# Kernel tuning notes

Measured on AMD Instinct MI355X. Metric: run time of the kernel, lower is better.

Reference implementation:

```python
import jax, jax.numpy as jnp
import numpy as np

B = 4096
D = 256
TEMP = 0.5


def setup_inputs() -> dict:
    key = jax.random.key(0)
    k1, k2 = jax.random.split(key)
    x_i = jax.random.normal(k1, (B, D), dtype=jnp.float32)
    x_j = jax.random.normal(k2, (B, D), dtype=jnp.float32)
    return {"x_i": x_i, "x_j": x_j}


def reference(x_i, x_j):
    b = x_i.shape[0]
    # L2-normalize rows (F.normalize with default eps=1e-12)
    def l2norm(x):
        n = jnp.linalg.norm(x, axis=1, keepdims=True)
        return x / jnp.maximum(n, 1e-12)

    z = jnp.concatenate([l2norm(x_i), l2norm(x_j)], axis=0)  # [2B, D]
    # rows of z are unit-norm, so cosine similarity == dot product
    sim = z @ z.T  # [2B, 2B]

    # positives: diagonals at offsets +B and -B
    idx = jnp.arange(b)
    sim_ij = sim[idx, idx + b]
    sim_ji = sim[idx + b, idx]
    pos = jnp.concatenate([sim_ij, sim_ji], axis=0)  # [2B]

    nom = jnp.exp(pos / TEMP)
    neg_mask = 1.0 - jnp.eye(2 * b, dtype=sim.dtype)
    denom = jnp.sum(neg_mask * jnp.exp(sim / TEMP), axis=1)  # [2B]
    loss = jnp.sum(-jnp.log(nom / denom)) / (2 * b)
    return loss
```

## Files before the change

kernel.cpp:

```cpp
#include <hip/hip_runtime.h>

#define NB   4096
#define ND   256
#define N2B  8192
#define INV_T 2.0f

typedef __attribute__((ext_vector_type(8))) short bf16x8;
typedef __attribute__((ext_vector_type(16))) float f32x16;

__device__ __forceinline__ void gload_lds16(const void* g, void* l) {
  __builtin_amdgcn_global_load_lds(
      (const __attribute__((address_space(1))) void*)g,
      (__attribute__((address_space(3))) void*)l, 16, 0, 0);
}

__device__ __forceinline__ unsigned short f2b(float f) {
  unsigned int u = __float_as_uint(f);
  u = (u + 0x7fffu + ((u >> 16) & 1u)) >> 16;
  return (unsigned short)u;
}
__device__ __forceinline__ float b2f(unsigned short h) {
  return __uint_as_float(((unsigned int)h) << 16);
}

__global__ __launch_bounds__(256) void k_normalize(
    const float* __restrict__ xi, const float* __restrict__ xj,
    unsigned short* __restrict__ Z, float* __restrict__ diagE,
    float* __restrict__ pos, float* __restrict__ lossAcc,
    unsigned int* __restrict__ ticket) {
  __shared__ float sh[2][256];
  if (blockIdx.x == 0 && threadIdx.x == 0) { *lossAcc = 0.0f; *ticket = 0u; }
  int wave = threadIdx.x >> 6, lane = threadIdx.x & 63;
  int r = (int)blockIdx.x * 2 + (wave & 1);
  bool isJ = wave >= 2;
  const float* src = (isJ ? xj : xi) + (size_t)r * ND;
  int zrow = r + (isJ ? NB : 0);

  float4 v = *(const float4*)(src + lane * 4);
  float ss = v.x * v.x + v.y * v.y + v.z * v.z + v.w * v.w;
#pragma unroll
  for (int m = 1; m < 64; m <<= 1) ss += __shfl_xor(ss, m, 64);
  float scale = 1.0f / fmaxf(sqrtf(ss), 1e-12f);
  unsigned short h0 = f2b(v.x * scale), h1 = f2b(v.y * scale);
  unsigned short h2 = f2b(v.z * scale), h3 = f2b(v.w * scale);
  ushort4 st; st.x = h0; st.y = h1; st.z = h2; st.w = h3;
  *(ushort4*)(Z + (size_t)zrow * ND + lane * 4) = st;

  float f0 = b2f(h0), f1 = b2f(h1), f2 = b2f(h2), f3 = b2f(h3);
  float d = f0 * f0 + f1 * f1 + f2 * f2 + f3 * f3;
#pragma unroll
  for (int m = 1; m < 64; m <<= 1) d += __shfl_xor(d, m, 64);
  if (lane == 0) diagE[zrow] = __expf(d * INV_T);

  if (isJ) {
    float* s = sh[wave & 1] + lane * 4;
    s[0] = f0; s[1] = f1; s[2] = f2; s[3] = f3;
  }
  __syncthreads();
  if (!isJ) {
    const float* s = sh[wave] + lane * 4;
    float p = f0 * s[0] + f1 * s[1] + f2 * s[2] + f3 * s[3];
#pragma unroll
    for (int m = 1; m < 64; m <<= 1) p += __shfl_xor(p, m, 64);
    if (lane == 0) pos[r] = p;
  }
}

__global__ __launch_bounds__(256, 2) void k_gemm_exp(
    const unsigned short* __restrict__ Z, float* __restrict__ R) {
  __shared__ alignas(16) unsigned short Bs[2][64 * ND];

  int tid = threadIdx.x;
  int wave = tid >> 6, lane = tid & 63;
  int r5 = lane & 31, h = lane >> 5;
  int band = (int)blockIdx.x >> 4;
  int span = (int)blockIdx.x & 15;
  int rowA = band * 256 + wave * 64;
  int colspan = span * 512;

  bf16x8 afr[2][16];
#pragma unroll
  for (int rg = 0; rg < 2; ++rg)
#pragma unroll
    for (int kk = 0; kk < 16; ++kk)
      afr[rg][kk] = *(const bf16x8*)(Z + (size_t)(rowA + rg * 32 + r5) * ND +
                                     kk * 16 + h * 8);

  float rs[2][16];
#pragma unroll
  for (int rg = 0; rg < 2; ++rg)
#pragma unroll
    for (int g = 0; g < 16; ++g) rs[rg][g] = 0.0f;

#define STAGE(t, b)                                                         \
  {                                                                         \
    int colbase = colspan + (t)*64;                                         \
    _Pragma("unroll") for (int call = 0; call < 8; ++call) {                \
      int r0 = wave * 16 + call * 2;                                        \
      int zr = colbase + r0 + h;                                            \
      int gc = r5 ^ (zr & 31);                                              \
      gload_lds16(Z + (size_t)zr * ND + gc * 8, &Bs[b][r0 * ND]);           \
    }                                                                       \
  }

  STAGE(0, 0)
  STAGE(1, 1)

#pragma unroll
  for (int t = 0; t < 8; ++t) {
    if (t < 7)
      asm volatile("s_waitcnt vmcnt(8)" ::: "memory");
    else
      asm volatile("s_waitcnt vmcnt(0)" ::: "memory");
    __syncthreads();

    const unsigned short* Bb = &Bs[t & 1][0];
#pragma unroll
    for (int ni = 0; ni < 2; ++ni) {
      f32x16 acc0 = {};
      f32x16 acc1 = {};
#pragma unroll
      for (int kk = 0; kk < 16; ++kk) {
        bf16x8 bf =
            *(const bf16x8*)&Bb[(ni * 32 + r5) * ND + (((kk * 2 + h) ^ r5) * 8)];
        acc0 = __builtin_amdgcn_mfma_f32_32x32x16_bf16(afr[0][kk], bf, acc0, 0,
                                                       0, 0);
        acc1 = __builtin_amdgcn_mfma_f32_32x32x16_bf16(afr[1][kk], bf, acc1, 0,
                                                       0, 0);
      }
#pragma unroll
      for (int g = 0; g < 16; ++g) {
        rs[0][g] += __expf(acc0[g] * INV_T);
        rs[1][g] += __expf(acc1[g] * INV_T);
      }
    }
    __syncthreads();
    if (t + 2 < 8) STAGE(t + 2, t & 1)
  }

#pragma unroll
  for (int m = 1; m <= 16; m <<= 1)
#pragma unroll
    for (int rg = 0; rg < 2; ++rg)
#pragma unroll
      for (int g = 0; g < 16; ++g)
        rs[rg][g] += __shfl_xor(rs[rg][g], m, 64);

#pragma unroll
  for (int rg = 0; rg < 2; ++rg)
#pragma unroll
    for (int g = 0; g < 16; ++g)
      if (r5 == g) {
        int rowIn = (g & 3) + 8 * (g >> 2) + 4 * h;
        R[(size_t)(rowA + rg * 32 + rowIn) * 16 + span] = rs[rg][g];
      }
#undef STAGE
}

__global__ __launch_bounds__(256) void k_final(
    const float* __restrict__ R, const float* __restrict__ diagE,
    const float* __restrict__ pos, float* __restrict__ lossAcc,
    unsigned int* __restrict__ ticket, float* __restrict__ out) {
  __shared__ float red[4];
  int tid = threadIdx.x;
  int wave = tid >> 6, lane = tid & 63;
  int row = (int)blockIdx.x * 256 + tid;

  const float* Rr = R + (size_t)row * 16;
  float s = -diagE[row];
#pragma unroll
  for (int i = 0; i < 4; ++i) {
    float4 a = *(const float4*)(Rr + i * 4);
    s += (a.x + a.y) + (a.z + a.w);
  }
  float term = __logf(s) - INV_T * pos[row & (NB - 1)];
#pragma unroll
  for (int m = 1; m < 64; m <<= 1) term += __shfl_xor(term, m, 64);
  if (lane == 0) red[wave] = term;
  __syncthreads();
  if (tid == 0) {
    float bs = red[0] + red[1] + red[2] + red[3];
    atomicAdd(lossAcc, bs);
    __threadfence();
    unsigned int old = atomicAdd(ticket, 1u);
    if (old == 31u) {
      float v = atomicAdd(lossAcc, 0.0f);
      out[0] = v * (1.0f / (float)N2B);
    }
  }
}

extern "C" void kernel_launch(void* const* d_in, const int* in_sizes, int n_in,
                              void* d_out, int out_size, void* d_ws,
                              size_t ws_size, hipStream_t stream) {
  const float* xi = (const float*)d_in[0];
  const float* xj = (const float*)d_in[1];
  float* out = (float*)d_out;
  char* ws = (char*)d_ws;
  unsigned short* Z = (unsigned short*)ws;
  float* R = (float*)(ws + (4u << 20));
  float* pos = (float*)(ws + (8u << 20));
  float* diagE = (float*)(ws + (8u << 20) + 65536);
  float* lossAcc = (float*)(ws + (8u << 20) + 131072);
  unsigned int* ticket = (unsigned int*)(ws + (8u << 20) + 131072 + 64);

  k_normalize<<<dim3(NB / 2), dim3(256), 0, stream>>>(xi, xj, Z, diagE, pos,
                                                      lossAcc, ticket);
  k_gemm_exp<<<dim3(512), dim3(256), 0, stream>>>(Z, R);
  k_final<<<dim3(32), dim3(256), 0, stream>>>(R, diagE, pos, lossAcc, ticket,
                                              out);
}
```

Measured before the change: 105.8 us.

## Drop LDS staging for B tiles and prescale A operand to use exp2

The GEMM kernel no longer stages B tiles through LDS with async global-to-LDS loads, double buffering and barriers. Each wave now reads its B fragments straight from global memory, relying on L2/L1 caching. The normalize kernel also writes a second copy of Z scaled by 2/ln2, so the epilogue can call exp2f directly instead of multiply-then-exp. The cost is an extra Z buffer write and a second rounding to bf16 on the scaled operand. Without LDS reuse across waves, memory latency may become exposed, because the g loop is not unrolled and has no explicit prefetch.

```diff
diff --git a/kernel.cpp b/kernel.cpp
--- a/kernel.cpp
+++ b/kernel.cpp
@@ -4,15 +4,10 @@
 #define ND   256
 #define N2B  8192
 #define INV_T 2.0f
+#define C_EXP 2.8853900817779268f
 
 typedef __attribute__((ext_vector_type(8))) short bf16x8;
 typedef __attribute__((ext_vector_type(16))) float f32x16;
-
-__device__ __forceinline__ void gload_lds16(const void* g, void* l) {
-  __builtin_amdgcn_global_load_lds(
-      (const __attribute__((address_space(1))) void*)g,
-      (__attribute__((address_space(3))) void*)l, 16, 0, 0);
-}
 
 __device__ __forceinline__ unsigned short f2b(float f) {
   unsigned int u = __float_as_uint(f);
@@ -25,9 +20,9 @@
 
 __global__ __launch_bounds__(256) void k_normalize(
     const float* __restrict__ xi, const float* __restrict__ xj,
-    unsigned short* __restrict__ Z, float* __restrict__ diagE,
-    float* __restrict__ pos, float* __restrict__ lossAcc,
-    unsigned int* __restrict__ ticket) {
+    unsigned short* __restrict__ Z, unsigned short* __restrict__ Zs,
+    float* __restrict__ diagE, float* __restrict__ pos,
+    float* __restrict__ lossAcc, unsigned int* __restrict__ ticket) {
   __shared__ float sh[2][256];
   if (blockIdx.x == 0 && threadIdx.x == 0) { *lossAcc = 0.0f; *ticket = 0u; }
   int wave = threadIdx.x >> 6, lane = threadIdx.x & 63;
@@ -47,6 +42,11 @@
   *(ushort4*)(Z + (size_t)zrow * ND + lane * 4) = st;
 
   float f0 = b2f(h0), f1 = b2f(h1), f2 = b2f(h2), f3 = b2f(h3);
+  ushort4 sts;
+  sts.x = f2b(f0 * C_EXP); sts.y = f2b(f1 * C_EXP);
+  sts.z = f2b(f2 * C_EXP); sts.w = f2b(f3 * C_EXP);
+  *(ushort4*)(Zs + (size_t)zrow * ND + lane * 4) = sts;
+
   float d = f0 * f0 + f1 * f1 + f2 * f2 + f3 * f3;
 #pragma unroll
   for (int m = 1; m < 64; m <<= 1) d += __shfl_xor(d, m, 64);
@@ -67,23 +67,21 @@
 }
 
 __global__ __launch_bounds__(256, 2) void k_gemm_exp(
-    const unsigned short* __restrict__ Z, float* __restrict__ R) {
-  __shared__ alignas(16) unsigned short Bs[2][64 * ND];
-
+    const unsigned short* __restrict__ Zs, const unsigned short* __restrict__ Z,
+    float* __restrict__ R) {
   int tid = threadIdx.x;
   int wave = tid >> 6, lane = tid & 63;
   int r5 = lane & 31, h = lane >> 5;
   int band = (int)blockIdx.x >> 4;
   int span = (int)blockIdx.x & 15;
   int rowA = band * 256 + wave * 64;
-  int colspan = span * 512;
 
   bf16x8 afr[2][16];
 #pragma unroll
   for (int rg = 0; rg < 2; ++rg)
 #pragma unroll
     for (int kk = 0; kk < 16; ++kk)
-      afr[rg][kk] = *(const bf16x8*)(Z + (size_t)(rowA + rg * 32 + r5) * ND +
+      afr[rg][kk] = *(const bf16x8*)(Zs + (size_t)(rowA + rg * 32 + r5) * ND +
                                      kk * 16 + h * 8);
 
   float rs[2][16];
@@ -92,50 +90,25 @@
 #pragma unroll
     for (int g = 0; g < 16; ++g) rs[rg][g] = 0.0f;
 
-#define STAGE(t, b)                                                         \
-  {                                                                         \
-    int colbase = colspan + (t)*64;                                         \
-    _Pragma("unroll") for (int call = 0; call < 8; ++call) {                \
-      int r0 = wave * 16 + call * 2;                                        \
-      int zr = colbase + r0 + h;                                            \
-      int gc = r5 ^ (zr & 31);                                              \
-      gload_lds16(Z + (size_t)zr * ND + gc * 8, &Bs[b][r0 * ND]);           \
-    }                                                                       \
-  }
+  const unsigned short* bbase = Z + (size_t)(span * 512 + r5) * ND + h * 8;
 
-  STAGE(0, 0)
-  STAGE(1, 1)
-
+  for (int g = 0; g < 16; ++g) {
+    const unsigned short* bp = bbase + (size_t)g * 32 * ND;
+    f32x16 acc0 = {};
+    f32x16 acc1 = {};
 #pragma unroll
-  for (int t = 0; t < 8; ++t) {
-    if (t < 7)
-      asm volatile("s_waitcnt vmcnt(8)" ::: "memory");
-    else
-      asm volatile("s_waitcnt vmcnt(0)" ::: "memory");
-    __syncthreads();
-
-    const unsigned short* Bb = &Bs[t & 1][0];
+    for (int kk = 0; kk < 16; ++kk) {
+      bf16x8 bf = *(const bf16x8*)(bp + kk * 16);
+      acc0 = __builtin_amdgcn_mfma_f32_32x32x16_bf16(afr[0][kk], bf, acc0, 0,
+                                                     0, 0);
+      acc1 = __builtin_amdgcn_mfma_f32_32x32x16_bf16(afr[1][kk], bf, acc1, 0,
+                                                     0, 0);
+    }
 #pragma unroll
-    for (int ni = 0; ni < 2; ++ni) {
-      f32x16 acc0 = {};
-      f32x16 acc1 = {};
-#pragma unroll
-      for (int kk = 0; kk < 16; ++kk) {
-        bf16x8 bf =
-            *(const bf16x8*)&Bb[(ni * 32 + r5) * ND + (((kk * 2 + h) ^ r5) * 8)];
-        acc0 = __builtin_amdgcn_mfma_f32_32x32x16_bf16(afr[0][kk], bf, acc0, 0,
-                                                       0, 0);
-        acc1 = __builtin_amdgcn_mfma_f32_32x32x16_bf16(afr[1][kk], bf, acc1, 0,
-                                                       0, 0);
-      }
-#pragma unroll
-      for (int g = 0; g < 16; ++g) {
-        rs[0][g] += __expf(acc0[g] * INV_T);
-        rs[1][g] += __expf(acc1[g] * INV_T);
-      }
+    for (int q = 0; q < 16; ++q) {
+      rs[0][q] += exp2f(acc0[q]);
+      rs[1][q] += exp2f(acc1[q]);
     }
-    __syncthreads();
-    if (t + 2 < 8) STAGE(t + 2, t & 1)
   }
 
 #pragma unroll
@@ -154,7 +127,6 @@
         int rowIn = (g & 3) + 8 * (g >> 2) + 4 * h;
         R[(size_t)(rowA + rg * 32 + rowIn) * 16 + span] = rs[rg][g];
       }
-#undef STAGE
 }
 
 __global__ __launch_bounds__(256) void k_final(
@@ -198,15 +170,16 @@
   float* out = (float*)d_out;
   char* ws = (char*)d_ws;
   unsigned short* Z = (unsigned short*)ws;
-  float* R = (float*)(ws + (4u << 20));
-  float* pos = (float*)(ws + (8u << 20));
-  float* diagE = (float*)(ws + (8u << 20) + 65536);
-  float* lossAcc = (float*)(ws + (8u << 20) + 131072);
-  unsigned int* ticket = (unsigned int*)(ws + (8u << 20) + 131072 + 64);
+  unsigned short* Zs = (unsigned short*)(ws + (4u << 20));
+  float* R = (float*)(ws + (8u << 20));
+  float* pos = (float*)(ws + (9u << 20));
+  float* diagE = (float*)(ws + (9u << 20) + 65536);
+  float* lossAcc = (float*)(ws + (9u << 20) + 131072);
+  unsigned int* ticket = (unsigned int*)(ws + (9u << 20) + 131072 + 64);
 
-  k_normalize<<<dim3(NB / 2), dim3(256), 0, stream>>>(xi, xj, Z, diagE, pos,
-                                                      lossAcc, ticket);
-  k_gemm_exp<<<dim3(512), dim3(256), 0, stream>>>(Z, R);
+  k_normalize<<<dim3(NB / 2), dim3(256), 0, stream>>>(xi, xj, Z, Zs, diagE,
+                                                      pos, lossAcc, ticket);
+  k_gemm_exp<<<dim3(512), dim3(256), 0, stream>>>(Zs, Z, R);
   k_final<<<dim3(32), dim3(256), 0, stream>>>(R, diagE, pos, lossAcc, ticket,
                                               out);
 }
```

After: 136.6 us. 1.29x slower.
